# Kernel optimization log

Hardware: AMD Instinct MI355X
Metric: run time of the kernel (lower is better)

Reference implementation:

```python
import jax, jax.numpy as jnp
import numpy as np

DIM = 128
NH = 4
K = 7
PAD = K // 2  # dilation = 1
MLP_HID = 4 * DIM
EPS = 1e-5


def _layernorm(x, w, b):
    m = jnp.mean(x, axis=-1, keepdims=True)
    v = jnp.mean((x - m) ** 2, axis=-1, keepdims=True)
    return (x - m) / jnp.sqrt(v + EPS) * w + b


def _windows(xp, H, W):
    # xp: [B, nh, Hp, Wp, hd] zero-padded; returns [B, nh, H, W, hd, K*K]
    return jnp.stack(
        [xp[:, :, i:i + H, j:j + W, :] for i in range(K) for j in range(K)],
        axis=-1,
    )


def setup_inputs() -> dict:
    key = jax.random.key(0)
    ks = jax.random.split(key, 10)
    s = 0.02
    inp = {
        "x": jax.random.normal(ks[0], (4, 56, 56, DIM), dtype=jnp.float32),
        "ln1_w": jnp.ones((DIM,), jnp.float32),
        "ln1_b": jnp.zeros((DIM,), jnp.float32),
        "w_qkv": jax.random.normal(ks[1], (DIM, 3 * DIM), jnp.float32) * s,
        "b_qkv": jnp.zeros((3 * DIM,), jnp.float32),
        "rpb": jax.random.normal(ks[2], (NH, K * K), jnp.float32) * s,
        "w_proj": jax.random.normal(ks[3], (DIM, DIM), jnp.float32) * s,
        "b_proj": jnp.zeros((DIM,), jnp.float32),
        "ln2_w": jnp.ones((DIM,), jnp.float32),
        "ln2_b": jnp.zeros((DIM,), jnp.float32),
        "w_fc1": jax.random.normal(ks[4], (DIM, MLP_HID), jnp.float32) * s,
        "b_fc1": jnp.zeros((MLP_HID,), jnp.float32),
        "w_fc2": jax.random.normal(ks[5], (MLP_HID, DIM), jnp.float32) * s,
        "b_fc2": jnp.zeros((DIM,), jnp.float32),
    }
    return inp


def _nat_block(x, ln1_w, ln1_b, w_qkv, b_qkv, rpb, w_proj, b_proj,
               ln2_w, ln2_b, w_fc1, b_fc1, w_fc2, b_fc2):
    B, H, W, C = x.shape
    hd = C // NH
    scale = hd ** -0.5

    # --- neighborhood attention ---
    xn = _layernorm(x, ln1_w, ln1_b)
    qkv = xn @ w_qkv + b_qkv                       # [B,H,W,3C]
    qkv = qkv.reshape(B, H, W, 3, NH, hd)
    qkv = jnp.transpose(qkv, (3, 0, 4, 1, 2, 5))   # [3,B,nh,H,W,hd]
    q, k, v = qkv[0] * scale, qkv[1], qkv[2]
    # zero-pad spatial dims (matches F.pad with constant 0 in original)
    pad = ((0, 0), (0, 0), (PAD, PAD), (PAD, PAD), (0, 0))
    kp = jnp.pad(k, pad)
    vp = jnp.pad(v, pad)
    kw = _windows(kp, H, W)                        # [B,nh,H,W,hd,49]
    vw = _windows(vp, H, W)
    attn = jnp.einsum('bnhwd,bnhwdk->bnhwk', q, kw)
    attn = attn + rpb[None, :, None, None, :]
    attn = jax.nn.softmax(attn, axis=-1)
    out = jnp.einsum('bnhwk,bnhwdk->bnhwd', attn, vw)  # [B,nh,H,W,hd]
    out = jnp.transpose(out, (0, 2, 3, 1, 4)).reshape(B, H, W, C)
    x = x + (out @ w_proj + b_proj)

    # --- MLP ---
    xn2 = _layernorm(x, ln2_w, ln2_b)
    h = jax.nn.gelu(xn2 @ w_fc1 + b_fc1, approximate=False)
    x = x + (h @ w_fc2 + b_fc2)
    return x


def reference(x, ln1_w, ln1_b, w_qkv, b_qkv, rpb, w_proj, b_proj,
              ln2_w, ln2_b, w_fc1, b_fc1, w_fc2, b_fc2):
    return _nat_block(x, ln1_w, ln1_b, w_qkv, b_qkv, rpb, w_proj, b_proj,
                      ln2_w, ln2_b, w_fc1, b_fc1, w_fc2, b_fc2)
```

## Files before the change

### kernel.cpp

```cpp
#include <hip/hip_runtime.h>

using bf16x8 = __attribute__((ext_vector_type(8))) short;
using f32x4  = __attribute__((ext_vector_type(4))) float;
typedef unsigned short u16;
typedef __attribute__((ext_vector_type(8))) unsigned short u16x8;

__device__ __forceinline__ u16 f2b(float f){
  unsigned int i=__float_as_uint(f);
  return (u16)((i + 0x7FFFu + ((i>>16)&1u))>>16);
}
__device__ __forceinline__ float b2f(u16 u){
  union{unsigned int i; float f;}v; v.i=((unsigned int)u)<<16; return v.f;
}
__device__ __forceinline__ void async16(const void* g, void* l){
  __builtin_amdgcn_global_load_lds((__attribute__((address_space(1))) void*)(g),
                                   (__attribute__((address_space(3))) void*)(l), 16, 0, 0);
}
__device__ __forceinline__ float gelu_tanh(float v){
  float u = v*(0.7978845608f + 0.0356774081f*v*v);
  float e = __expf(-2.0f*fabsf(u));
  float th = (1.0f-e)/(1.0f+e);
  th = (u<0.f)? -th : th;
  return 0.5f*v*(1.0f+th);
}

__global__ void prep_kernel(const float* __restrict__ wqkv, const float* __restrict__ wproj,
                            const float* __restrict__ wfc1, const float* __restrict__ wfc2,
                            u16* __restrict__ tqkv, u16* __restrict__ tproj,
                            u16* __restrict__ tfc1, u16* __restrict__ tfc2,
                            u16* __restrict__ vb3)
{
  int idx = blockIdx.x*256 + threadIdx.x;
  if (idx < 49152){
    int nc = idx>>14, r = idx&16383, i = r>>3, e = r&7, n = i&127, c = i>>7;
    tqkv[idx] = f2b(wqkv[(c*8+e)*384 + nc*128 + n]);
  } else if (idx < 65536){
    int r = idx-49152; int i=r>>3, e=r&7, n=i&127, c=i>>7;
    tproj[r] = f2b(wproj[(c*8+e)*128 + n]);
  } else if (idx < 131072){
    int t = idx-65536; int nc=t>>14, r=t&16383, i=r>>3, e=r&7, n=i&127, c=i>>7;
    tfc1[t] = f2b(wfc1[(c*8+e)*512 + nc*128 + n]);
  } else if (idx < 196608){
    int t = idx-131072; int nc=t>>14, r=t&16383, i=r>>3, e=r&7, n=i&127, c=i>>7;
    tfc2[t] = f2b(wfc2[(nc*128 + c*8 + e)*128 + n]);
  } else {
    int zi = idx - 196608;
    u16x8 z = {0,0,0,0,0,0,0,0};
    ((u16x8*)vb3)[zi] = z;
  }
}


__global__ __launch_bounds__(256)
void qkv_ln_kernel(const float* __restrict__ x,
                   const float* __restrict__ ln1w, const float* __restrict__ ln1b,
                   const u16* __restrict__ tqkv, const float* __restrict__ bqkv,
                   u16* __restrict__ qb, u16* __restrict__ kb, u16* __restrict__ vb3)
{
  __shared__ __align__(16) char smem[40960];
  char* lA = smem;
  char* lB = smem + 8192;

  const int tid = threadIdx.x;
  const int lane = tid&63, wid = tid>>6;
  const int quad = lane>>4, lrow = lane&15;
  const int m0 = blockIdx.x*32;
  const int nc = blockIdx.y;
  const int wm = (wid&1)*16, wn = (wid>>1)*64;

  #pragma unroll
  for (int kk=0;kk<8;kk++){
    int i = tid + kk*256;
    async16(tqkv + (size_t)nc*16384 + i*8, lB + i*16);
  }

  {
    const int row = tid>>3, g = tid&7;
    float xv[16];
    const float4* xr = (const float4*)(x + (size_t)(m0+row)*128 + g*16);
    float s=0.f, sq=0.f;
    #pragma unroll
    for (int c4=0;c4<4;c4++){
      float4 t = xr[c4];
      xv[c4*4]=t.x; xv[c4*4+1]=t.y; xv[c4*4+2]=t.z; xv[c4*4+3]=t.w;
      s += t.x+t.y+t.z+t.w;
      sq += t.x*t.x+t.y*t.y+t.z*t.z+t.w*t.w;
    }
    s  += __shfl_xor(s,1);  s  += __shfl_xor(s,2);  s  += __shfl_xor(s,4);
    sq += __shfl_xor(sq,1); sq += __shfl_xor(sq,2); sq += __shfl_xor(sq,4);
    float mean = s*0.0078125f;
    float rstd = rsqrtf(sq*0.0078125f - mean*mean + 1e-5f);
    const float4* wr = (const float4*)(ln1w + g*16);
    const float4* br = (const float4*)(ln1b + g*16);
    u16 nv[16];
    #pragma unroll
    for (int c4=0;c4<4;c4++){
      float4 w4 = wr[c4], b4 = br[c4];
      nv[c4*4]   = f2b((xv[c4*4]  -mean)*rstd*w4.x + b4.x);
      nv[c4*4+1] = f2b((xv[c4*4+1]-mean)*rstd*w4.y + b4.y);
      nv[c4*4+2] = f2b((xv[c4*4+2]-mean)*rstd*w4.z + b4.z);
      nv[c4*4+3] = f2b((xv[c4*4+3]-mean)*rstd*w4.w + b4.w);
    }
    #pragma unroll
    for (int cc=0;cc<2;cc++){
      u16x8 pk;
      #pragma unroll
      for (int e=0;e<8;e++) pk[e] = nv[cc*8+e];
      *(u16x8*)(lA + (((g*2+cc)*32 + row)<<4)) = pk;
    }
  }
  __syncthreads();

  f32x4 acc[4] = {};
  #pragma unroll
  for (int ks=0;ks<4;ks++){
    bf16x8 af = ((const bf16x8*)lA)[(ks*4+quad)*32 + wm + lrow];
    #pragma unroll
    for (int j=0;j<4;j++){
      bf16x8 bfr = ((const bf16x8*)lB)[(ks*4+quad)*128 + wn + j*16 + lrow];
      acc[j] = __builtin_amdgcn_mfma_f32_16x16x32_bf16(af, bfr, acc[j], 0,0,0);
    }
  }

  const float scale = 0.17677669529663687f;
  #pragma unroll
  for (int j=0;j<4;j++){
    int col = wn + j*16 + lrow;
    float bia = bqkv[nc*128 + col];
    #pragma unroll
    for (int r=0;r<4;r++){
      int row = m0 + wm + quad*4 + r;
      float val = acc[j][r] + bia;
      if (nc==0){
        qb[(size_t)row*128 + col] = f2b(val*scale);
      } else if (nc==1){
        kb[(size_t)row*128 + col] = f2b(val);
      } else {
        int hh = col>>5, ch = col&31;
        int bq = row/3136, rem = row - bq*3136;
        int yy = rem/56, xx = rem - yy*56;
        vb3[(size_t)(((bq*4+hh)*32 + ch)<<12) + (yy+3)*64 + (xx+3)] = f2b(val);
      }
    }
  }
}

#define KT_S 40
#define VT_S 232
#define P_S  152
__global__ __launch_bounds__(256)
void attn_kernel(const u16* __restrict__ qb, const u16* __restrict__ kb,
                 const u16* __restrict__ vb3, const float* __restrict__ rpb,
                 u16* __restrict__ aout)
{
  __shared__ __align__(16) char smem[52424];
  u16*  kt   = (u16*)smem;
  u16*  vt   = (u16*)(smem + 17920);
  u16*  Pm   = (u16*)(smem + 32768);
  float* srpb= (float*)(smem + 52224);

  const int tid = threadIdx.x;
  const int tile = blockIdx.x, bh = blockIdx.y;
  const int b = bh>>2, h = bh&3;
  const int ty = (tile/7)*8, tx = (tile%7)*8;
  const int lane = tid&63, wid = tid>>6;
  const int quad = lane>>4, lrow = lane&15;

  #pragma unroll
  for (int kk=0;kk<4;kk++){
    int i = tid + kk*256;
    if (i < 896){
      int pos16 = i>>2, oct = i&3;
      int hx = pos16&15, hy = pos16>>4;
      if (hx < 14){
        int gy = ty+hy-3, gx = tx+hx-3;
        u16x8 kv = {0,0,0,0,0,0,0,0};
        if ((unsigned)gy<56u && (unsigned)gx<56u)
          kv = *(const u16x8*)(kb + ((size_t)(b*3136 + gy*56 + gx)*128 + h*32 + oct*8));
        *(u16x8*)(kt + pos16*KT_S + oct*8) = kv;
      }
    }
  }
  #pragma unroll
  for (int kk=0;kk<4;kk++){
    int i = tid + kk*256;
    if (i < 896){
      int lo = i&1, t2 = i>>1;
      int ch = t2/14, hy = t2 - ch*14;
      *(u16x8*)(vt + ch*VT_S + hy*16 + lo*8) =
        *(const u16x8*)(vb3 + ((size_t)(bh*32 + ch)<<12) + (ty+hy)*64 + tx + lo*8);
    }
  }
  if (tid < 49) srpb[tid] = rpb[h*49 + tid];
  __syncthreads();

  const int pxq = wid*16 + lrow;
  const int tokq = b*3136 + (ty + (pxq>>3))*56 + tx + (pxq&7);
  bf16x8 qf = *(const bf16x8*)(qb + (size_t)tokq*128 + h*32 + quad*8);

  f32x4 sc[8];
  const f32x4 zf = {0.f,0.f,0.f,0.f};
  #pragma unroll
  for (int cg=0;cg<8;cg++){
    bf16x8 kf = *(const bf16x8*)(kt + (wid*32 + cg*16 + lrow)*KT_S + quad*8);
    sc[cg] = __builtin_amdgcn_mfma_f32_16x16x32_bf16(qf, kf, zf, 0,0,0);
  }

  const int lyq = quad>>1;
  #pragma unroll
  for (int cg=0;cg<8;cg++){
    int dy = cg - lyq;
    bool rowok = ((unsigned)dy < 7u) && (lrow < 14);
    #pragma unroll
    for (int r=0;r<4;r++){
      int lx = (quad*4+r)&7;
      int dx = lrow - lx;
      bool in = rowok && ((unsigned)dx < 7u);
      float bias = srpb[in ? (dy*7+dx) : 0];
      sc[cg][r] = in ? (sc[cg][r] + bias) : -1e30f;
    }
  }
  float inv[4];
  #pragma unroll
  for (int r=0;r<4;r++){
    float m = sc[0][r];
    #pragma unroll
    for (int cg=1;cg<8;cg++) m = fmaxf(m, sc[cg][r]);
    m = fmaxf(m, __shfl_xor(m,1)); m = fmaxf(m, __shfl_xor(m,2));
    m = fmaxf(m, __shfl_xor(m,4)); m = fmaxf(m, __shfl_xor(m,8));
    float l = 0.f;
    #pragma unroll
    for (int cg=0;cg<8;cg++){ float p = __expf(sc[cg][r]-m); sc[cg][r]=p; l+=p; }
    l += __shfl_xor(l,1); l += __shfl_xor(l,2);
    l += __shfl_xor(l,4); l += __shfl_xor(l,8);
    inv[r]=1.f/l;
  }

  u16* Pw = Pm + wid*16*P_S;
  #pragma unroll
  for (int cg=0;cg<8;cg++){
    #pragma unroll
    for (int r=0;r<4;r++)
      Pw[(quad*4+r)*P_S + cg*16 + lrow] = f2b(sc[cg][r]);
  }

  f32x4 oacc[2] = {zf, zf};
  #pragma unroll
  for (int ks=0;ks<4;ks++){
    bf16x8 pf = *(const bf16x8*)(Pw + lrow*P_S + ks*32 + quad*8);
    #pragma unroll
    for (int cg2=0;cg2<2;cg2++){
      bf16x8 vf = *(const bf16x8*)(vt + (cg2*16+lrow)*VT_S + wid*32 + ks*32 + quad*8);
      oacc[cg2] = __builtin_amdgcn_mfma_f32_16x16x32_bf16(pf, vf, oacc[cg2], 0,0,0);
    }
  }
  #pragma unroll
  for (int r=0;r<4;r++){
    int px = wid*16 + quad*4 + r;
    int tok = b*3136 + (ty + (px>>3))*56 + tx + (px&7);
    #pragma unroll
    for (int cg2=0;cg2<2;cg2++){
      int ch = h*32 + cg2*16 + lrow;
      aout[(size_t)((tok>>5)*16 + (ch>>3))*256 + (tok&31)*8 + (ch&7)]
        = f2b(oacc[cg2][r]*inv[r]);
    }
  }
}

__global__ __launch_bounds__(256)
void mega_mlp_kernel(const u16* __restrict__ aout, const float* __restrict__ x,
                     const u16* __restrict__ tproj, const float* __restrict__ bproj,
                     const float* __restrict__ ln2w, const float* __restrict__ ln2b,
                     const u16* __restrict__ tfc1, const float* __restrict__ bfc1,
                     const u16* __restrict__ tfc2, const float* __restrict__ bfc2,
                     float* __restrict__ out)
{
  __shared__ __align__(16) char smem[49664];
  char* lA  = smem;
  char* lB  = smem + 8192;
  char* xn2 = smem + 40960;
  float* redS = (float*)(smem + 49152);
  float* redQ = redS + 64;

  const int tid = threadIdx.x;
  const int lane = tid&63, wid = tid>>6;
  const int quad = lane>>4, lrow = lane&15;
  const int m0 = blockIdx.x*32;
  const int wm = (wid&1)*16, wn = (wid>>1)*64;
  const int half = wid>>1;

  #pragma unroll
  for (int kk=0;kk<2;kk++){
    int i = tid + kk*256;
    async16(aout + (size_t)blockIdx.x*4096 + i*8, lA + i*16);
  }
  #pragma unroll
  for (int kk=0;kk<8;kk++){
    int i = tid + kk*256;
    async16(tproj + (size_t)i*8, lB + i*16);
  }
  __syncthreads();

  f32x4 acc[4] = {};
  #pragma unroll
  for (int ks=0;ks<4;ks++){
    bf16x8 af = ((const bf16x8*)lA)[(ks*4+quad)*32 + wm + lrow];
    #pragma unroll
    for (int j=0;j<4;j++){
      bf16x8 bfr = ((const bf16x8*)lB)[(ks*4+quad)*128 + wn + j*16 + lrow];
      acc[j] = __builtin_amdgcn_mfma_f32_16x16x32_bf16(af, bfr, acc[j], 0,0,0);
    }
  }

  float x1v[4][4];
  float ps[4] = {}, pq[4] = {};
  #pragma unroll
  for (int j=0;j<4;j++){
    int col = wn + j*16 + lrow;
    float bia = bproj[col];
    #pragma unroll
    for (int r=0;r<4;r++){
      int row = m0 + wm + quad*4 + r;
      float val = acc[j][r] + bia + x[(size_t)row*128 + col];
      x1v[j][r] = val;
      ps[r] += val; pq[r] += val*val;
    }
  }
  #pragma unroll
  for (int r=0;r<4;r++){
    #pragma unroll
    for (int off=1; off<16; off<<=1){
      ps[r] += __shfl_xor(ps[r], off);
      pq[r] += __shfl_xor(pq[r], off);
    }
  }
  if (lrow==0){
    #pragma unroll
    for (int r=0;r<4;r++){
      int row = wm + quad*4 + r;
      redS[half*32 + row] = ps[r];
      redQ[half*32 + row] = pq[r];
    }
  }
  __syncthreads();

  {
    float w2[4], b2[4];
    #pragma unroll
    for (int j=0;j<4;j++){ int col = wn+j*16+lrow; w2[j]=ln2w[col]; b2[j]=ln2b[col]; }
    #pragma unroll
    for (int r=0;r<4;r++){
      int row = wm + quad*4 + r;
      float mean = (redS[row] + redS[32+row])*0.0078125f;
      float var  = (redQ[row] + redQ[32+row])*0.0078125f - mean*mean;
      float rstd = rsqrtf(var + 1e-5f);
      #pragma unroll
      for (int j=0;j<4;j++){
        int col = wn + j*16 + lrow;
        u16 hv = f2b((x1v[j][r]-mean)*rstd*w2[j] + b2[j]);
        ((u16*)xn2)[((col>>3)*32 + row)*8 + (col&7)] = hv;
      }
    }
  }
  __syncthreads();

  f32x4 acc3[4] = {};
  for (int nc=0; nc<4; nc++){
    if (nc>0) __syncthreads();
    #pragma unroll
    for (int kk=0;kk<8;kk++){
      int i = tid + kk*256;
      async16(tfc1 + (size_t)nc*16384 + i*8, lB + i*16);
    }
    __syncthreads();

    f32x4 acc2[4] = {};
    #pragma unroll
    for (int ks=0;ks<4;ks++){
      bf16x8 af = ((const bf16x8*)xn2)[(ks*4+quad)*32 + wm + lrow];
      #pragma unroll
      for (int j=0;j<4;j++){
        bf16x8 bfr = ((const bf16x8*)lB)[(ks*4+quad)*128 + wn + j*16 + lrow];
        acc2[j] = __builtin_amdgcn_mfma_f32_16x16x32_bf16(af, bfr, acc2[j], 0,0,0);
      }
    }
    #pragma unroll
    for (int j=0;j<4;j++){
      int col = wn + j*16 + lrow;
      float bia = bfc1[nc*128 + col];
      #pragma unroll
      for (int r=0;r<4;r++){
        int row = wm + quad*4 + r;
        float g = gelu_tanh(acc2[j][r] + bia);
        ((u16*)lA)[((col>>3)*32 + row)*8 + (col&7)] = f2b(g);
      }
    }
    __syncthreads();
    #pragma unroll
    for (int kk=0;kk<8;kk++){
      int i = tid + kk*256;
      async16(tfc2 + (size_t)nc*16384 + i*8, lB + i*16);
    }
    __syncthreads();

    #pragma unroll
    for (int ks=0;ks<4;ks++){
      bf16x8 af = ((const bf16x8*)lA)[(ks*4+quad)*32 + wm + lrow];
      #pragma unroll
      for (int j=0;j<4;j++){
        bf16x8 bfr = ((const bf16x8*)lB)[(ks*4+quad)*128 + wn + j*16 + lrow];
        acc3[j] = __builtin_amdgcn_mfma_f32_16x16x32_bf16(af, bfr, acc3[j], 0,0,0);
      }
    }
  }

  #pragma unroll
  for (int j=0;j<4;j++){
    int col = wn + j*16 + lrow;
    float bia = bfc2[col];
    #pragma unroll
    for (int r=0;r<4;r++){
      int row = m0 + wm + quad*4 + r;
      out[(size_t)row*128 + col] = acc3[j][r] + bia + x1v[j][r];
    }
  }
}

extern "C" void kernel_launch(void* const* d_in, const int* in_sizes, int n_in,
                              void* d_out, int out_size, void* d_ws, size_t ws_size,
                              hipStream_t stream)
{
  const float* x     =(const float*)d_in[0];
  const float* ln1w  =(const float*)d_in[1];
  const float* ln1b  =(const float*)d_in[2];
  const float* wqkv  =(const float*)d_in[3];
  const float* bqkv  =(const float*)d_in[4];
  const float* rpb   =(const float*)d_in[5];
  const float* wproj =(const float*)d_in[6];
  const float* bproj =(const float*)d_in[7];
  const float* ln2w  =(const float*)d_in[8];
  const float* ln2b  =(const float*)d_in[9];
  const float* wfc1  =(const float*)d_in[10];
  const float* bfc1  =(const float*)d_in[11];
  const float* wfc2  =(const float*)d_in[12];
  const float* bfc2  =(const float*)d_in[13];

  char* ws=(char*)d_ws;
  size_t o=0;
  u16* tqkv =(u16*)(ws+o); o+=98304;
  u16* tproj=(u16*)(ws+o); o+=32768;
  u16* tfc1 =(u16*)(ws+o); o+=131072;
  u16* tfc2 =(u16*)(ws+o); o+=131072;
  u16* aout =(u16*)(ws+o); o+=3211264;
  u16* qb   =(u16*)(ws+o); o+=3211264;
  u16* kb   =(u16*)(ws+o); o+=3211264;
  u16* vb3  =(u16*)(ws+o); o+=4194304;

  prep_kernel<<<1792,256,0,stream>>>(wqkv,wproj,wfc1,wfc2,tqkv,tproj,tfc1,tfc2,vb3);
  qkv_ln_kernel<<<dim3(392,3),256,0,stream>>>(x,ln1w,ln1b,tqkv,bqkv,qb,kb,vb3);
  attn_kernel<<<dim3(49,16),256,0,stream>>>(qb,kb,vb3,rpb,aout);
  mega_mlp_kernel<<<392,256,0,stream>>>(aout,x,tproj,bproj,ln2w,ln2b,
                                        tfc1,bfc1,tfc2,bfc2,(float*)d_out);
}
```

Baseline: 133.3 us.

## Fuse QKV, attention and MLP kernels into one cooperative persistent kernel

Merges the three compute kernels into a single cooperative kernel. It loops over tiles grid-stride and uses grid.sync between the QKV, attention and MLP phases. This is meant to remove kernel launch overhead and inter-kernel gaps. In exchange, the persistent grid of 512 blocks may use fewer CUs or waves than the original grids, and the grid-wide barriers cost time. The old three-kernel path remains as a fallback if the cooperative launch fails.

```diff
diff --git a/kernel.cpp b/kernel.cpp
--- a/kernel.cpp
+++ b/kernel.cpp
@@ -1,4 +1,7 @@
 #include <hip/hip_runtime.h>
+#include <hip/hip_cooperative_groups.h>
+
+namespace cg = cooperative_groups;
 
 using bf16x8 = __attribute__((ext_vector_type(8))) short;
 using f32x4  = __attribute__((ext_vector_type(4))) float;
@@ -8,9 +11,6 @@
 __device__ __forceinline__ u16 f2b(float f){
   unsigned int i=__float_as_uint(f);
   return (u16)((i + 0x7FFFu + ((i>>16)&1u))>>16);
-}
-__device__ __forceinline__ float b2f(u16 u){
-  union{unsigned int i; float f;}v; v.i=((unsigned int)u)<<16; return v.f;
 }
 __device__ __forceinline__ void async16(const void* g, void* l){
   __builtin_amdgcn_global_load_lds((__attribute__((address_space(1))) void*)(g),
@@ -50,48 +50,52 @@
   }
 }
 
-
-__global__ __launch_bounds__(256)
-void qkv_ln_kernel(const float* __restrict__ x,
-                   const float* __restrict__ ln1w, const float* __restrict__ ln1b,
-                   const u16* __restrict__ tqkv, const float* __restrict__ bqkv,
-                   u16* __restrict__ qb, u16* __restrict__ kb, u16* __restrict__ vb3)
+struct Params {
+  const float* x; const float* ln1w; const float* ln1b;
+  const u16* tqkv; const float* bqkv; const float* rpb;
+  const u16* tproj; const float* bproj; const float* ln2w; const float* ln2b;
+  const u16* tfc1; const float* bfc1; const u16* tfc2; const float* bfc2;
+  u16* qb; u16* kb; u16* vb3; u16* aout; float* out;
+};
+
+#define KT_S 40
+#define VT_S 232
+#define P_S  152
+
+__device__ __forceinline__ void phase1_tile(const Params& p, int t, char* smem,
+                                            int tid, int wid, int quad, int lrow)
 {
-  __shared__ __align__(16) char smem[40960];
   char* lA = smem;
   char* lB = smem + 8192;
-
-  const int tid = threadIdx.x;
-  const int lane = tid&63, wid = tid>>6;
-  const int quad = lane>>4, lrow = lane&15;
-  const int m0 = blockIdx.x*32;
-  const int nc = blockIdx.y;
   const int wm = (wid&1)*16, wn = (wid>>1)*64;
+  const int nc = t / 392;
+  const int m0 = (t - nc*392) * 32;
+  __syncthreads();
 
   #pragma unroll
   for (int kk=0;kk<8;kk++){
     int i = tid + kk*256;
-    async16(tqkv + (size_t)nc*16384 + i*8, lB + i*16);
+    async16(p.tqkv + (size_t)nc*16384 + i*8, lB + i*16);
   }
 
   {
     const int row = tid>>3, g = tid&7;
     float xv[16];
-    const float4* xr = (const float4*)(x + (size_t)(m0+row)*128 + g*16);
+    const float4* xr = (const float4*)(p.x + (size_t)(m0+row)*128 + g*16);
     float s=0.f, sq=0.f;
     #pragma unroll
     for (int c4=0;c4<4;c4++){
-      float4 t = xr[c4];
-      xv[c4*4]=t.x; xv[c4*4+1]=t.y; xv[c4*4+2]=t.z; xv[c4*4+3]=t.w;
-      s += t.x+t.y+t.z+t.w;
-      sq += t.x*t.x+t.y*t.y+t.z*t.z+t.w*t.w;
+      float4 tt = xr[c4];
+      xv[c4*4]=tt.x; xv[c4*4+1]=tt.y; xv[c4*4+2]=tt.z; xv[c4*4+3]=tt.w;
+      s += tt.x+tt.y+tt.z+tt.w;
+      sq += tt.x*tt.x+tt.y*tt.y+tt.z*tt.z+tt.w*tt.w;
     }
     s  += __shfl_xor(s,1);  s  += __shfl_xor(s,2);  s  += __shfl_xor(s,4);
     sq += __shfl_xor(sq,1); sq += __shfl_xor(sq,2); sq += __shfl_xor(sq,4);
     float mean = s*0.0078125f;
     float rstd = rsqrtf(sq*0.0078125f - mean*mean + 1e-5f);
-    const float4* wr = (const float4*)(ln1w + g*16);
-    const float4* br = (const float4*)(ln1b + g*16);
+    const float4* wr = (const float4*)(p.ln1w + g*16);
+    const float4* br = (const float4*)(p.ln1b + g*16);
     u16 nv[16];
     #pragma unroll
     for (int c4=0;c4<4;c4++){
@@ -123,48 +127,53 @@
   }
 
   const float scale = 0.17677669529663687f;
-  #pragma unroll
-  for (int j=0;j<4;j++){
-    int col = wn + j*16 + lrow;
-    float bia = bqkv[nc*128 + col];
+  if (nc < 2){
+    u16* dst = (nc==0)? p.qb : p.kb;
+    #pragma unroll
+    for (int j=0;j<4;j++){
+      int col = wn + j*16 + lrow;
+      float bia = p.bqkv[nc*128 + col];
+      #pragma unroll
+      for (int r=0;r<4;r++){
+        int row = m0 + wm + quad*4 + r;
+        float val = acc[j][r] + bia;
+        if (nc==0) val *= scale;
+        dst[(size_t)row*128 + col] = f2b(val);
+      }
+    }
+  } else {
+    int row0 = m0 + wm + quad*4;
+    int bq = row0/3136, rem = row0 - bq*3136;
+    int yy = rem/56, xx = rem - yy*56;
+    float bia[4];
+    #pragma unroll
+    for (int j=0;j<4;j++) bia[j] = p.bqkv[256 + wn + j*16 + lrow];
     #pragma unroll
     for (int r=0;r<4;r++){
-      int row = m0 + wm + quad*4 + r;
-      float val = acc[j][r] + bia;
-      if (nc==0){
-        qb[(size_t)row*128 + col] = f2b(val*scale);
-      } else if (nc==1){
-        kb[(size_t)row*128 + col] = f2b(val);
-      } else {
+      size_t pbase = (size_t)(yy+3)*64 + (xx+3);
+      #pragma unroll
+      for (int j=0;j<4;j++){
+        int col = wn + j*16 + lrow;
         int hh = col>>5, ch = col&31;
-        int bq = row/3136, rem = row - bq*3136;
-        int yy = rem/56, xx = rem - yy*56;
-        vb3[(size_t)(((bq*4+hh)*32 + ch)<<12) + (yy+3)*64 + (xx+3)] = f2b(val);
-      }
-    }
-  }
-}
-
-#define KT_S 40
-#define VT_S 232
-#define P_S  152
-__global__ __launch_bounds__(256)
-void attn_kernel(const u16* __restrict__ qb, const u16* __restrict__ kb,
-                 const u16* __restrict__ vb3, const float* __restrict__ rpb,
-                 u16* __restrict__ aout)
+        p.vb3[((size_t)(((bq<<2)+hh)*32 + ch)<<12) + pbase] = f2b(acc[j][r] + bia[j]);
+      }
+      xx++;
+      if (xx==56){ xx=0; yy++; if (yy==56){ yy=0; bq++; } }
+    }
+  }
+}
+
+__device__ __forceinline__ void phase2_tile(const Params& p, int t, char* smem,
+                                            int tid, int wid, int quad, int lrow)
 {
-  __shared__ __align__(16) char smem[52424];
   u16*  kt   = (u16*)smem;
   u16*  vt   = (u16*)(smem + 17920);
   u16*  Pm   = (u16*)(smem + 32768);
   float* srpb= (float*)(smem + 52224);
-
-  const int tid = threadIdx.x;
-  const int tile = blockIdx.x, bh = blockIdx.y;
+  const int bh = t / 49, tile = t - bh*49;
   const int b = bh>>2, h = bh&3;
   const int ty = (tile/7)*8, tx = (tile%7)*8;
-  const int lane = tid&63, wid = tid>>6;
-  const int quad = lane>>4, lrow = lane&15;
+  __syncthreads();
 
   #pragma unroll
   for (int kk=0;kk<4;kk++){
@@ -176,7 +185,7 @@
         int gy = ty+hy-3, gx = tx+hx-3;
         u16x8 kv = {0,0,0,0,0,0,0,0};
         if ((unsigned)gy<56u && (unsigned)gx<56u)
-          kv = *(const u16x8*)(kb + ((size_t)(b*3136 + gy*56 + gx)*128 + h*32 + oct*8));
+          kv = *(const u16x8*)(p.kb + ((size_t)(b*3136 + gy*56 + gx)*128 + h*32 + oct*8));
         *(u16x8*)(kt + pos16*KT_S + oct*8) = kv;
       }
     }
@@ -188,15 +197,15 @@
       int lo = i&1, t2 = i>>1;
       int ch = t2/14, hy = t2 - ch*14;
       *(u16x8*)(vt + ch*VT_S + hy*16 + lo*8) =
-        *(const u16x8*)(vb3 + ((size_t)(bh*32 + ch)<<12) + (ty+hy)*64 + tx + lo*8);
-    }
-  }
-  if (tid < 49) srpb[tid] = rpb[h*49 + tid];
+        *(const u16x8*)(p.vb3 + ((size_t)(bh*32 + ch)<<12) + (ty+hy)*64 + tx + lo*8);
+    }
+  }
+  if (tid < 49) srpb[tid] = p.rpb[h*49 + tid];
   __syncthreads();
 
   const int pxq = wid*16 + lrow;
   const int tokq = b*3136 + (ty + (pxq>>3))*56 + tx + (pxq&7);
-  bf16x8 qf = *(const bf16x8*)(qb + (size_t)tokq*128 + h*32 + quad*8);
+  bf16x8 qf = *(const bf16x8*)(p.qb + (size_t)tokq*128 + h*32 + quad*8);
 
   f32x4 sc[8];
   const f32x4 zf = {0.f,0.f,0.f,0.f};
@@ -230,7 +239,7 @@
     m = fmaxf(m, __shfl_xor(m,4)); m = fmaxf(m, __shfl_xor(m,8));
     float l = 0.f;
     #pragma unroll
-    for (int cg=0;cg<8;cg++){ float p = __expf(sc[cg][r]-m); sc[cg][r]=p; l+=p; }
+    for (int cg=0;cg<8;cg++){ float pp = __expf(sc[cg][r]-m); sc[cg][r]=pp; l+=pp; }
     l += __shfl_xor(l,1); l += __shfl_xor(l,2);
     l += __shfl_xor(l,4); l += __shfl_xor(l,8);
     inv[r]=1.f/l;
@@ -261,43 +270,34 @@
     #pragma unroll
     for (int cg2=0;cg2<2;cg2++){
       int ch = h*32 + cg2*16 + lrow;
-      aout[(size_t)((tok>>5)*16 + (ch>>3))*256 + (tok&31)*8 + (ch&7)]
+      p.aout[(size_t)((tok>>5)*16 + (ch>>3))*256 + (tok&31)*8 + (ch&7)]
         = f2b(oacc[cg2][r]*inv[r]);
     }
   }
 }
 
-__global__ __launch_bounds__(256)
-void mega_mlp_kernel(const u16* __restrict__ aout, const float* __restrict__ x,
-                     const u16* __restrict__ tproj, const float* __restrict__ bproj,
-                     const float* __restrict__ ln2w, const float* __restrict__ ln2b,
-                     const u16* __restrict__ tfc1, const float* __restrict__ bfc1,
-                     const u16* __restrict__ tfc2, const float* __restrict__ bfc2,
-                     float* __restrict__ out)
+__device__ __forceinline__ void phase3_tile(const Params& p, int t, char* smem,
+                                            int tid, int wid, int quad, int lrow)
 {
-  __shared__ __align__(16) char smem[49664];
   char* lA  = smem;
   char* lB  = smem + 8192;
   char* xn2 = smem + 40960;
   float* redS = (float*)(smem + 49152);
   float* redQ = redS + 64;
-
-  const int tid = threadIdx.x;
-  const int lane = tid&63, wid = tid>>6;
-  const int quad = lane>>4, lrow = lane&15;
-  const int m0 = blockIdx.x*32;
   const int wm = (wid&1)*16, wn = (wid>>1)*64;
   const int half = wid>>1;
+  const int m0 = t*32;
+  __syncthreads();
 
   #pragma unroll
   for (int kk=0;kk<2;kk++){
     int i = tid + kk*256;
-    async16(aout + (size_t)blockIdx.x*4096 + i*8, lA + i*16);
+    async16(p.aout + (size_t)t*4096 + i*8, lA + i*16);
   }
   #pragma unroll
   for (int kk=0;kk<8;kk++){
     int i = tid + kk*256;
-    async16(tproj + (size_t)i*8, lB + i*16);
+    async16(p.tproj + (size_t)i*8, lB + i*16);
   }
   __syncthreads();
 
@@ -317,11 +317,11 @@
   #pragma unroll
   for (int j=0;j<4;j++){
     int col = wn + j*16 + lrow;
-    float bia = bproj[col];
+    float bia = p.bproj[col];
     #pragma unroll
     for (int r=0;r<4;r++){
       int row = m0 + wm + quad*4 + r;
-      float val = acc[j][r] + bia + x[(size_t)row*128 + col];
+      float val = acc[j][r] + bia + p.x[(size_t)row*128 + col];
       x1v[j][r] = val;
       ps[r] += val; pq[r] += val*val;
     }
@@ -347,7 +347,7 @@
   {
     float w2[4], b2[4];
     #pragma unroll
-    for (int j=0;j<4;j++){ int col = wn+j*16+lrow; w2[j]=ln2w[col]; b2[j]=ln2b[col]; }
+    for (int j=0;j<4;j++){ int col = wn+j*16+lrow; w2[j]=p.ln2w[col]; b2[j]=p.ln2b[col]; }
     #pragma unroll
     for (int r=0;r<4;r++){
       int row = wm + quad*4 + r;
@@ -370,7 +370,7 @@
     #pragma unroll
     for (int kk=0;kk<8;kk++){
       int i = tid + kk*256;
-      async16(tfc1 + (size_t)nc*16384 + i*8, lB + i*16);
+      async16(p.tfc1 + (size_t)nc*16384 + i*8, lB + i*16);
     }
     __syncthreads();
 
@@ -387,7 +387,7 @@
     #pragma unroll
     for (int j=0;j<4;j++){
       int col = wn + j*16 + lrow;
-      float bia = bfc1[nc*128 + col];
+      float bia = p.bfc1[nc*128 + col];
       #pragma unroll
       for (int r=0;r<4;r++){
         int row = wm + quad*4 + r;
@@ -399,7 +399,7 @@
     #pragma unroll
     for (int kk=0;kk<8;kk++){
       int i = tid + kk*256;
-      async16(tfc2 + (size_t)nc*16384 + i*8, lB + i*16);
+      async16(p.tfc2 + (size_t)nc*16384 + i*8, lB + i*16);
     }
     __syncthreads();
 
@@ -417,13 +417,47 @@
   #pragma unroll
   for (int j=0;j<4;j++){
     int col = wn + j*16 + lrow;
-    float bia = bfc2[col];
+    float bia = p.bfc2[col];
     #pragma unroll
     for (int r=0;r<4;r++){
       int row = m0 + wm + quad*4 + r;
-      out[(size_t)row*128 + col] = acc3[j][r] + bia + x1v[j][r];
-    }
-  }
+      p.out[(size_t)row*128 + col] = acc3[j][r] + bia + x1v[j][r];
+    }
+  }
+}
+
+__global__ __launch_bounds__(256) void qkv_kernel(Params p){
+  __shared__ __align__(16) char smem[40960];
+  int tid=threadIdx.x, lane=tid&63, wid=tid>>6, quad=lane>>4, lrow=lane&15;
+  phase1_tile(p, blockIdx.x, smem, tid, wid, quad, lrow);
+}
+__global__ __launch_bounds__(256) void attn_kernel(Params p){
+  __shared__ __align__(16) char smem[52480];
+  int tid=threadIdx.x, lane=tid&63, wid=tid>>6, quad=lane>>4, lrow=lane&15;
+  phase2_tile(p, blockIdx.x, smem, tid, wid, quad, lrow);
+}
+__global__ __launch_bounds__(256) void mega_kernel(Params p){
+  __shared__ __align__(16) char smem[49664];
+  int tid=threadIdx.x, lane=tid&63, wid=tid>>6, quad=lane>>4, lrow=lane&15;
+  phase3_tile(p, blockIdx.x, smem, tid, wid, quad, lrow);
+}
+
+__global__ __launch_bounds__(256) void fused_kernel(Params p){
+  __shared__ __align__(16) char smem[52480];
+  cg::grid_group grid = cg::this_grid();
+  int tid=threadIdx.x, lane=tid&63, wid=tid>>6, quad=lane>>4, lrow=lane&15;
+  int gs = gridDim.x;
+
+  for (int t = blockIdx.x; t < 1176; t += gs)
+    phase1_tile(p, t, smem, tid, wid, quad, lrow);
+  __threadfence();
+  grid.sync();
+  for (int t = blockIdx.x; t < 784; t += gs)
+    phase2_tile(p, t, smem, tid, wid, quad, lrow);
+  __threadfence();
+  grid.sync();
+  for (int t = blockIdx.x; t < 392; t += gs)
+    phase3_tile(p, t, smem, tid, wid, quad, lrow);
 }
 
 extern "C" void kernel_launch(void* const* d_in, const int* in_sizes, int n_in,
@@ -457,8 +491,24 @@
   u16* vb3  =(u16*)(ws+o); o+=4194304;
 
   prep_kernel<<<1792,256,0,stream>>>(wqkv,wproj,wfc1,wfc2,tqkv,tproj,tfc1,tfc2,vb3);
-  qkv_ln_kernel<<<dim3(392,3),256,0,stream>>>(x,ln1w,ln1b,tqkv,bqkv,qb,kb,vb3);
-  attn_kernel<<<dim3(49,16),256,0,stream>>>(qb,kb,vb3,rpb,aout);
-  mega_mlp_kernel<<<392,256,0,stream>>>(aout,x,tproj,bproj,ln2w,ln2b,
-                                        tfc1,bfc1,tfc2,bfc2,(float*)d_out);
-}
+
+  Params prm;
+  prm.x=x; prm.ln1w=ln1w; prm.ln1b=ln1b;
+  prm.tqkv=tqkv; prm.bqkv=bqkv; prm.rpb=rpb;
+  prm.tproj=tproj; prm.bproj=bproj; prm.ln2w=ln2w; prm.ln2b=ln2b;
+  prm.tfc1=tfc1; prm.bfc1=bfc1; prm.tfc2=tfc2; prm.bfc2=bfc2;
+  prm.qb=qb; prm.kb=kb; prm.vb3=vb3; prm.aout=aout; prm.out=(float*)d_out;
+
+  void* args[] = { &prm };
+  hipError_t e = hipLaunchCooperativeKernel((const void*)fused_kernel, dim3(512),
+                                            dim3(256), args, 0, stream);
+  if (e != hipSuccess){
+    e = hipLaunchCooperativeKernel((const void*)fused_kernel, dim3(256),
+                                   dim3(256), args, 0, stream);
+  }
+  if (e != hipSuccess){
+    qkv_kernel <<<1176,256,0,stream>>>(prm);
+    attn_kernel<<< 784,256,0,stream>>>(prm);
+    mega_kernel<<< 392,256,0,stream>>>(prm);
+  }
+}
```

Result: slower. 396.2 us (+197.1%).

## Halve MLP row tile, reuse attention LDS for P, hoist V index math

Applied to the files above, without the earlier changes.

The fused proj+MLP kernel now processes 16 rows per block instead of 32, across 784 blocks, with each wave owning 32 output columns. Its LN2 reduction goes through four per-wave partials stored in reused LDS, and shared memory drops from about 49KB to 40KB. The attention kernel stores the softmax probabilities into the K-tile region after a barrier instead of a separate buffer, cutting LDS to about 33KB to raise occupancy. The V scatter in the QKV kernel computes the row-to-(b,y,x) division once and increments it, avoiding per-element divides. The cost is more blocks, each reloading the full fc1/fc2 weights, plus an extra barrier in attention.

```diff
diff --git a/kernel.cpp b/kernel.cpp
--- a/kernel.cpp
+++ b/kernel.cpp
@@ -8,9 +8,6 @@
 __device__ __forceinline__ u16 f2b(float f){
   unsigned int i=__float_as_uint(f);
   return (u16)((i + 0x7FFFu + ((i>>16)&1u))>>16);
-}
-__device__ __forceinline__ float b2f(u16 u){
-  union{unsigned int i; float f;}v; v.i=((unsigned int)u)<<16; return v.f;
 }
 __device__ __forceinline__ void async16(const void* g, void* l){
   __builtin_amdgcn_global_load_lds((__attribute__((address_space(1))) void*)(g),
@@ -52,10 +49,10 @@
 
 
 __global__ __launch_bounds__(256)
-void qkv_ln_kernel(const float* __restrict__ x,
-                   const float* __restrict__ ln1w, const float* __restrict__ ln1b,
-                   const u16* __restrict__ tqkv, const float* __restrict__ bqkv,
-                   u16* __restrict__ qb, u16* __restrict__ kb, u16* __restrict__ vb3)
+void qkv_kernel(const float* __restrict__ x,
+                const float* __restrict__ ln1w, const float* __restrict__ ln1b,
+                const u16* __restrict__ tqkv, const float* __restrict__ bqkv,
+                u16* __restrict__ qb, u16* __restrict__ kb, u16* __restrict__ vb3)
 {
   __shared__ __align__(16) char smem[40960];
   char* lA = smem;
@@ -81,10 +78,10 @@
     float s=0.f, sq=0.f;
     #pragma unroll
     for (int c4=0;c4<4;c4++){
-      float4 t = xr[c4];
-      xv[c4*4]=t.x; xv[c4*4+1]=t.y; xv[c4*4+2]=t.z; xv[c4*4+3]=t.w;
-      s += t.x+t.y+t.z+t.w;
-      sq += t.x*t.x+t.y*t.y+t.z*t.z+t.w*t.w;
+      float4 tt = xr[c4];
+      xv[c4*4]=tt.x; xv[c4*4+1]=tt.y; xv[c4*4+2]=tt.z; xv[c4*4+3]=tt.w;
+      s += tt.x+tt.y+tt.z+tt.w;
+      sq += tt.x*tt.x+tt.y*tt.y+tt.z*tt.z+tt.w*tt.w;
     }
     s  += __shfl_xor(s,1);  s  += __shfl_xor(s,2);  s  += __shfl_xor(s,4);
     sq += __shfl_xor(sq,1); sq += __shfl_xor(sq,2); sq += __shfl_xor(sq,4);
@@ -123,41 +120,54 @@
   }
 
   const float scale = 0.17677669529663687f;
-  #pragma unroll
-  for (int j=0;j<4;j++){
-    int col = wn + j*16 + lrow;
-    float bia = bqkv[nc*128 + col];
-    #pragma unroll
-    for (int r=0;r<4;r++){
-      int row = m0 + wm + quad*4 + r;
-      float val = acc[j][r] + bia;
-      if (nc==0){
-        qb[(size_t)row*128 + col] = f2b(val*scale);
-      } else if (nc==1){
-        kb[(size_t)row*128 + col] = f2b(val);
-      } else {
+  if (nc < 2){
+    u16* dst = (nc==0)? qb : kb;
+    #pragma unroll
+    for (int j=0;j<4;j++){
+      int col = wn + j*16 + lrow;
+      float bia = bqkv[nc*128 + col];
+      #pragma unroll
+      for (int r=0;r<4;r++){
+        int row = m0 + wm + quad*4 + r;
+        float val = acc[j][r] + bia;
+        if (nc==0) val *= scale;
+        dst[(size_t)row*128 + col] = f2b(val);
+      }
+    }
+  } else {
+    int row0 = m0 + wm + quad*4;
+    int bq = row0/3136, rem = row0 - bq*3136;
+    int yy = rem/56, xx = rem - yy*56;
+    float bia[4];
+    #pragma unroll
+    for (int j=0;j<4;j++) bia[j] = bqkv[256 + wn + j*16 + lrow];
+    #pragma unroll
+    for (int r=0;r<4;r++){
+      size_t pbase = (size_t)(yy+3)*64 + (xx+3);
+      #pragma unroll
+      for (int j=0;j<4;j++){
+        int col = wn + j*16 + lrow;
         int hh = col>>5, ch = col&31;
-        int bq = row/3136, rem = row - bq*3136;
-        int yy = rem/56, xx = rem - yy*56;
-        vb3[(size_t)(((bq*4+hh)*32 + ch)<<12) + (yy+3)*64 + (xx+3)] = f2b(val);
-      }
+        vb3[((size_t)(((bq<<2)+hh)*32 + ch)<<12) + pbase] = f2b(acc[j][r] + bia[j]);
+      }
+      xx++;
+      if (xx==56){ xx=0; yy++; if (yy==56){ yy=0; bq++; } }
     }
   }
 }
 
 #define KT_S 40
 #define VT_S 232
-#define P_S  152
+#define P_S  136
 __global__ __launch_bounds__(256)
 void attn_kernel(const u16* __restrict__ qb, const u16* __restrict__ kb,
                  const u16* __restrict__ vb3, const float* __restrict__ rpb,
                  u16* __restrict__ aout)
 {
-  __shared__ __align__(16) char smem[52424];
+  __shared__ __align__(16) char smem[33024];
   u16*  kt   = (u16*)smem;
   u16*  vt   = (u16*)(smem + 17920);
-  u16*  Pm   = (u16*)(smem + 32768);
-  float* srpb= (float*)(smem + 52224);
+  float* srpb= (float*)(smem + 32768);
 
   const int tid = threadIdx.x;
   const int tile = blockIdx.x, bh = blockIdx.y;
@@ -230,13 +240,14 @@
     m = fmaxf(m, __shfl_xor(m,4)); m = fmaxf(m, __shfl_xor(m,8));
     float l = 0.f;
     #pragma unroll
-    for (int cg=0;cg<8;cg++){ float p = __expf(sc[cg][r]-m); sc[cg][r]=p; l+=p; }
+    for (int cg=0;cg<8;cg++){ float pp = __expf(sc[cg][r]-m); sc[cg][r]=pp; l+=pp; }
     l += __shfl_xor(l,1); l += __shfl_xor(l,2);
     l += __shfl_xor(l,4); l += __shfl_xor(l,8);
     inv[r]=1.f/l;
   }
 
-  u16* Pw = Pm + wid*16*P_S;
+  __syncthreads();
+  u16* Pw = kt + wid*16*P_S;
   #pragma unroll
   for (int cg=0;cg<8;cg++){
     #pragma unroll
@@ -268,32 +279,28 @@
 }
 
 __global__ __launch_bounds__(256)
-void mega_mlp_kernel(const u16* __restrict__ aout, const float* __restrict__ x,
-                     const u16* __restrict__ tproj, const float* __restrict__ bproj,
-                     const float* __restrict__ ln2w, const float* __restrict__ ln2b,
-                     const u16* __restrict__ tfc1, const float* __restrict__ bfc1,
-                     const u16* __restrict__ tfc2, const float* __restrict__ bfc2,
-                     float* __restrict__ out)
+void mega_kernel(const u16* __restrict__ aout, const float* __restrict__ x,
+                 const u16* __restrict__ tproj, const float* __restrict__ bproj,
+                 const float* __restrict__ ln2w, const float* __restrict__ ln2b,
+                 const u16* __restrict__ tfc1, const float* __restrict__ bfc1,
+                 const u16* __restrict__ tfc2, const float* __restrict__ bfc2,
+                 float* __restrict__ out)
 {
-  __shared__ __align__(16) char smem[49664];
+  __shared__ __align__(16) char smem[40960];
   char* lA  = smem;
-  char* lB  = smem + 8192;
-  char* xn2 = smem + 40960;
-  float* redS = (float*)(smem + 49152);
-  float* redQ = redS + 64;
+  char* lB  = smem + 4096;
+  char* xn2 = smem + 36864;
 
   const int tid = threadIdx.x;
   const int lane = tid&63, wid = tid>>6;
   const int quad = lane>>4, lrow = lane&15;
-  const int m0 = blockIdx.x*32;
-  const int wm = (wid&1)*16, wn = (wid>>1)*64;
-  const int half = wid>>1;
-
-  #pragma unroll
-  for (int kk=0;kk<2;kk++){
-    int i = tid + kk*256;
-    async16(aout + (size_t)blockIdx.x*4096 + i*8, lA + i*16);
-  }
+  const int t = blockIdx.x;
+  const int m0 = t*16;
+  const int g = t>>1, off = (t&1)*16;
+  const int wn = wid*32;
+
+  { int i = tid; int c = i>>4, row = i&15;
+    async16(aout + (size_t)(g*16 + c)*256 + (off+row)*8, lA + i*16); }
   #pragma unroll
   for (int kk=0;kk<8;kk++){
     int i = tid + kk*256;
@@ -301,26 +308,26 @@
   }
   __syncthreads();
 
-  f32x4 acc[4] = {};
+  f32x4 acc[2] = {};
   #pragma unroll
   for (int ks=0;ks<4;ks++){
-    bf16x8 af = ((const bf16x8*)lA)[(ks*4+quad)*32 + wm + lrow];
-    #pragma unroll
-    for (int j=0;j<4;j++){
+    bf16x8 af = ((const bf16x8*)lA)[(ks*4+quad)*16 + lrow];
+    #pragma unroll
+    for (int j=0;j<2;j++){
       bf16x8 bfr = ((const bf16x8*)lB)[(ks*4+quad)*128 + wn + j*16 + lrow];
       acc[j] = __builtin_amdgcn_mfma_f32_16x16x32_bf16(af, bfr, acc[j], 0,0,0);
     }
   }
 
-  float x1v[4][4];
+  float x1v[2][4];
   float ps[4] = {}, pq[4] = {};
   #pragma unroll
-  for (int j=0;j<4;j++){
+  for (int j=0;j<2;j++){
     int col = wn + j*16 + lrow;
     float bia = bproj[col];
     #pragma unroll
     for (int r=0;r<4;r++){
-      int row = m0 + wm + quad*4 + r;
+      int row = m0 + quad*4 + r;
       float val = acc[j][r] + bia + x[(size_t)row*128 + col];
       x1v[j][r] = val;
       ps[r] += val; pq[r] += val*val;
@@ -329,42 +336,47 @@
   #pragma unroll
   for (int r=0;r<4;r++){
     #pragma unroll
-    for (int off=1; off<16; off<<=1){
-      ps[r] += __shfl_xor(ps[r], off);
-      pq[r] += __shfl_xor(pq[r], off);
-    }
-  }
+    for (int o2=1; o2<16; o2<<=1){
+      ps[r] += __shfl_xor(ps[r], o2);
+      pq[r] += __shfl_xor(pq[r], o2);
+    }
+  }
+  __syncthreads();
+  float* redS = (float*)lA;
+  float* redQ = redS + 64;
   if (lrow==0){
     #pragma unroll
     for (int r=0;r<4;r++){
-      int row = wm + quad*4 + r;
-      redS[half*32 + row] = ps[r];
-      redQ[half*32 + row] = pq[r];
+      int row = quad*4 + r;
+      redS[wid*16 + row] = ps[r];
+      redQ[wid*16 + row] = pq[r];
     }
   }
   __syncthreads();
 
   {
-    float w2[4], b2[4];
-    #pragma unroll
-    for (int j=0;j<4;j++){ int col = wn+j*16+lrow; w2[j]=ln2w[col]; b2[j]=ln2b[col]; }
-    #pragma unroll
-    for (int r=0;r<4;r++){
-      int row = wm + quad*4 + r;
-      float mean = (redS[row] + redS[32+row])*0.0078125f;
-      float var  = (redQ[row] + redQ[32+row])*0.0078125f - mean*mean;
+    float w2[2], b2[2];
+    #pragma unroll
+    for (int j=0;j<2;j++){ int col = wn+j*16+lrow; w2[j]=ln2w[col]; b2[j]=ln2b[col]; }
+    #pragma unroll
+    for (int r=0;r<4;r++){
+      int row = quad*4 + r;
+      float s = redS[row] + redS[16+row] + redS[32+row] + redS[48+row];
+      float q = redQ[row] + redQ[16+row] + redQ[32+row] + redQ[48+row];
+      float mean = s*0.0078125f;
+      float var  = q*0.0078125f - mean*mean;
       float rstd = rsqrtf(var + 1e-5f);
       #pragma unroll
-      for (int j=0;j<4;j++){
+      for (int j=0;j<2;j++){
         int col = wn + j*16 + lrow;
         u16 hv = f2b((x1v[j][r]-mean)*rstd*w2[j] + b2[j]);
-        ((u16*)xn2)[((col>>3)*32 + row)*8 + (col&7)] = hv;
-      }
-    }
-  }
-  __syncthreads();
-
-  f32x4 acc3[4] = {};
+        ((u16*)xn2)[((col>>3)*16 + row)*8 + (col&7)] = hv;
+      }
+    }
+  }
+  __syncthreads();
+
+  f32x4 acc3[2] = {};
   for (int nc=0; nc<4; nc++){
     if (nc>0) __syncthreads();
     #pragma unroll
@@ -374,25 +386,25 @@
     }
     __syncthreads();
 
-    f32x4 acc2[4] = {};
+    f32x4 acc2[2] = {};
     #pragma unroll
     for (int ks=0;ks<4;ks++){
-      bf16x8 af = ((const bf16x8*)xn2)[(ks*4+quad)*32 + wm + lrow];
-      #pragma unroll
-      for (int j=0;j<4;j++){
+      bf16x8 af = ((const bf16x8*)xn2)[(ks*4+quad)*16 + lrow];
+      #pragma unroll
+      for (int j=0;j<2;j++){
         bf16x8 bfr = ((const bf16x8*)lB)[(ks*4+quad)*128 + wn + j*16 + lrow];
         acc2[j] = __builtin_amdgcn_mfma_f32_16x16x32_bf16(af, bfr, acc2[j], 0,0,0);
       }
     }
     #pragma unroll
-    for (int j=0;j<4;j++){
+    for (int j=0;j<2;j++){
       int col = wn + j*16 + lrow;
       float bia = bfc1[nc*128 + col];
       #pragma unroll
       for (int r=0;r<4;r++){
-        int row = wm + quad*4 + r;
-        float g = gelu_tanh(acc2[j][r] + bia);
-        ((u16*)lA)[((col>>3)*32 + row)*8 + (col&7)] = f2b(g);
+        int row = quad*4 + r;
+        float gg = gelu_tanh(acc2[j][r] + bia);
+        ((u16*)lA)[((col>>3)*16 + row)*8 + (col&7)] = f2b(gg);
       }
     }
     __syncthreads();
@@ -405,9 +417,9 @@
 
     #pragma unroll
     for (int ks=0;ks<4;ks++){
-      bf16x8 af = ((const bf16x8*)lA)[(ks*4+quad)*32 + wm + lrow];
-      #pragma unroll
-      for (int j=0;j<4;j++){
+      bf16x8 af = ((const bf16x8*)lA)[(ks*4+quad)*16 + lrow];
+      #pragma unroll
+      for (int j=0;j<2;j++){
         bf16x8 bfr = ((const bf16x8*)lB)[(ks*4+quad)*128 + wn + j*16 + lrow];
         acc3[j] = __builtin_amdgcn_mfma_f32_16x16x32_bf16(af, bfr, acc3[j], 0,0,0);
       }
@@ -415,12 +427,12 @@
   }
 
   #pragma unroll
-  for (int j=0;j<4;j++){
+  for (int j=0;j<2;j++){
     int col = wn + j*16 + lrow;
     float bia = bfc2[col];
     #pragma unroll
     for (int r=0;r<4;r++){
-      int row = m0 + wm + quad*4 + r;
+      int row = m0 + quad*4 + r;
       out[(size_t)row*128 + col] = acc3[j][r] + bia + x1v[j][r];
     }
   }
@@ -457,8 +469,8 @@
   u16* vb3  =(u16*)(ws+o); o+=4194304;
 
   prep_kernel<<<1792,256,0,stream>>>(wqkv,wproj,wfc1,wfc2,tqkv,tproj,tfc1,tfc2,vb3);
-  qkv_ln_kernel<<<dim3(392,3),256,0,stream>>>(x,ln1w,ln1b,tqkv,bqkv,qb,kb,vb3);
+  qkv_kernel<<<dim3(392,3),256,0,stream>>>(x,ln1w,ln1b,tqkv,bqkv,qb,kb,vb3);
   attn_kernel<<<dim3(49,16),256,0,stream>>>(qb,kb,vb3,rpb,aout);
-  mega_mlp_kernel<<<392,256,0,stream>>>(aout,x,tproj,bproj,ln2w,ln2b,
-                                        tfc1,bfc1,tfc2,bfc2,(float*)d_out);
-}
+  mega_kernel<<<784,256,0,stream>>>(aout,x,tproj,bproj,ln2w,ln2b,
+                                    tfc1,bfc1,tfc2,bfc2,(float*)d_out);
+}
```

Measured after the change: 131.0 us. About the same (-1.8%).
